# Kernel tuning notes

Hardware: AMD Instinct MI355X
Metric: run time of the kernel (lower is better)

Reference implementation:

```python
import jax, jax.numpy as jnp
import numpy as np

ALPHA = 0.25
GAMMA = 2.0
EPS_CLIP = 1e-4


def calc_iou(a, b):
    # a: [A,4] anchors, b: [M,4] gt boxes, boxes are [x1,y1,x2,y2]
    area = (b[:, 2] - b[:, 0]) * (b[:, 3] - b[:, 1])  # [M]
    iw = jnp.minimum(a[:, None, 2], b[None, :, 2]) - jnp.maximum(a[:, None, 0], b[None, :, 0])
    ih = jnp.minimum(a[:, None, 3], b[None, :, 3]) - jnp.maximum(a[:, None, 1], b[None, :, 1])
    iw = jnp.maximum(iw, 0.0)
    ih = jnp.maximum(ih, 0.0)
    ua = ((a[:, 2] - a[:, 0]) * (a[:, 3] - a[:, 1]))[:, None] + area[None, :] - iw * ih
    ua = jnp.maximum(ua, 1e-8)
    return iw * ih / ua  # [A,M]


def _per_image(cls_p, reg_p, ann, anchor):
    # cls_p [A,C], reg_p [A,4], ann [M,5], anchor [A,4]
    aw = anchor[:, 2] - anchor[:, 0]
    ah = anchor[:, 3] - anchor[:, 1]
    acx = anchor[:, 0] + 0.5 * aw
    acy = anchor[:, 1] + 0.5 * ah

    valid = ann[:, 4] != -1.0            # [M] padding mask
    has_ann = jnp.any(valid)

    cls_p = jnp.clip(cls_p, EPS_CLIP, 1.0 - EPS_CLIP)

    iou = calc_iou(anchor, ann[:, :4])   # [A,M]
    iou = jnp.where(valid[None, :], iou, -1.0)  # invalid gt never matched
    iou_max = jnp.max(iou, axis=1)       # [A]
    iou_arg = jnp.argmax(iou, axis=1)    # [A]
    assigned = ann[iou_arg]              # [A,5]

    neg = iou_max < 0.4
    pos = iou_max >= 0.5
    num_pos = jnp.sum(pos.astype(jnp.float32))

    C = cls_p.shape[1]
    targets = jnp.full_like(cls_p, -1.0)
    targets = jnp.where(neg[:, None], 0.0, targets)
    targets = jnp.where(pos[:, None], 0.0, targets)
    cls_idx = assigned[:, 4].astype(jnp.int32)
    onehot = (jnp.arange(C)[None, :] == cls_idx[:, None]) & pos[:, None]
    targets = jnp.where(onehot, 1.0, targets)

    alpha_f = jnp.where(targets == 1.0, ALPHA, 1.0 - ALPHA)
    focal_w = alpha_f * jnp.where(targets == 1.0, 1.0 - cls_p, cls_p) ** GAMMA
    bce = -(targets * jnp.log(cls_p) + (1.0 - targets) * jnp.log(1.0 - cls_p))
    cls_loss = jnp.where(targets != -1.0, focal_w * bce, 0.0)
    cls_l = jnp.where(has_ann, jnp.sum(cls_loss) / jnp.maximum(num_pos, 1.0), 0.0)

    gw0 = assigned[:, 2] - assigned[:, 0]
    gh0 = assigned[:, 3] - assigned[:, 1]
    gcx = assigned[:, 0] + 0.5 * gw0
    gcy = assigned[:, 1] + 0.5 * gh0
    gw = jnp.maximum(gw0, 1.0)
    gh = jnp.maximum(gh0, 1.0)
    tdx = (gcx - acx) / aw
    tdy = (gcy - acy) / ah
    tdw = jnp.log(gw / aw)
    tdh = jnp.log(gh / ah)
    norm = jnp.array([0.1, 0.1, 0.2, 0.2], dtype=cls_p.dtype)
    rt = jnp.stack([tdx, tdy, tdw, tdh], axis=1) / norm  # [A,4]

    diff = jnp.abs(rt - reg_p)
    sl1 = jnp.where(diff <= 1.0 / 9.0, 0.5 * 9.0 * diff * diff, diff - 0.5 / 9.0)
    reg_sum = jnp.sum(sl1 * pos[:, None].astype(sl1.dtype))
    reg_l = jnp.where(has_ann & (num_pos > 0), reg_sum / jnp.maximum(num_pos * 4.0, 1.0), 0.0)
    return cls_l, reg_l


def setup_inputs() -> dict:
    key = jax.random.key(0)
    ks = jax.random.split(key, 10)
    B, A, C, M = 8, 49104, 90, 32
    IMG = 512.0

    classifications = jax.random.uniform(ks[0], (B, A, C), dtype=jnp.float32)
    regressions = jax.random.normal(ks[1], (B, A, 4), dtype=jnp.float32)

    # anchors: valid boxes [x1,y1,x2,y2]
    acx = jax.random.uniform(ks[2], (A,), minval=0.0, maxval=IMG)
    acy = jax.random.uniform(ks[3], (A,), minval=0.0, maxval=IMG)
    asz = jax.random.uniform(ks[4], (A, 2), minval=16.0, maxval=128.0)
    anchors = jnp.stack([acx - 0.5 * asz[:, 0], acy - 0.5 * asz[:, 1],
                         acx + 0.5 * asz[:, 0], acy + 0.5 * asz[:, 1]], axis=1)[None].astype(jnp.float32)

    # annotations: [x1,y1,x2,y2,label], label=-1 marks padding
    gx1 = jax.random.uniform(ks[5], (B, M), minval=0.0, maxval=IMG - 64.0)
    gy1 = jax.random.uniform(ks[6], (B, M), minval=0.0, maxval=IMG - 64.0)
    gwh = jax.random.uniform(ks[7], (B, M, 2), minval=16.0, maxval=64.0)
    labels = jax.random.randint(ks[8], (B, M), 0, C).astype(jnp.float32)
    invalid = jax.random.uniform(ks[9], (B, M)) < 0.25
    labels = jnp.where(invalid, -1.0, labels)
    labels = labels.at[:, 0].set(jnp.abs(labels[:, 0]))  # ensure >=1 valid gt per image
    annotations = jnp.concatenate([gx1[..., None], gy1[..., None],
                                   (gx1 + gwh[..., 0])[..., None],
                                   (gy1 + gwh[..., 1])[..., None],
                                   labels[..., None]], axis=-1).astype(jnp.float32)

    return {"classifications": classifications, "regressions": regressions,
            "anchors": anchors, "annotations": annotations}


def reference(classifications, regressions, anchors, annotations):
    cls_l, reg_l = jax.vmap(_per_image, in_axes=(0, 0, 0, None))(
        classifications, regressions, annotations, anchors[0])
    return (jnp.mean(cls_l, keepdims=True), jnp.mean(reg_l, keepdims=True))
```

## Files before the change

kernel.cpp:

```cpp
#include <hip/hip_runtime.h>

constexpr int B = 8;
constexpr int A = 49104;
constexpr int C = 90;
constexpr int M = 32;
constexpr float EPS_CLIP = 1e-4f;
constexpr float LN2 = 0.6931471805599453f;

constexpr int APB = 256;
constexpr int TPB = 256;
constexpr int UN  = 8;


__global__ __launch_bounds__(TPB, 6) void focal_fused_kernel(
    const float* __restrict__ cls,
    const float* __restrict__ reg,
    const float* __restrict__ anc,
    const float* __restrict__ ann,
    float* __restrict__ accum)
{
    __shared__ float s_ann[M * 5];
    __shared__ int   s_meta[APB + 1];
    __shared__ float s_red[3][TPB / 64];

    const int b     = blockIdx.y;
    const int abase = blockIdx.x * APB;
    const int t     = threadIdx.x;
    const int nA    = min(APB, A - abase);

    if (t < M * 5) s_ann[t] = ann[b * M * 5 + t];
    __syncthreads();

    float reg_sum = 0.f;
    float pos_cnt = 0.f;
    int   mymeta  = -1;

    if (t < nA) {
        const int a = abase + t;
        const float4 ab = reinterpret_cast<const float4*>(anc)[a];
        const float aw = ab.z - ab.x;
        const float ah = ab.w - ab.y;
        const float areaA = aw * ah;

        float best = -INFINITY;
        int argm = 0;
        for (int m = 0; m < M; ++m) {
            const float bx1 = s_ann[m * 5 + 0];
            const float by1 = s_ann[m * 5 + 1];
            const float bx2 = s_ann[m * 5 + 2];
            const float by2 = s_ann[m * 5 + 3];
            const float lab = s_ann[m * 5 + 4];
            float iw = fminf(ab.z, bx2) - fmaxf(ab.x, bx1);
            float ih = fminf(ab.w, by2) - fmaxf(ab.y, by1);
            iw = fmaxf(iw, 0.f);
            ih = fmaxf(ih, 0.f);
            const float inter = iw * ih;
            const float ua = fmaxf(areaA + (bx2 - bx1) * (by2 - by1) - inter, 1e-8f);
            const float iou = inter / ua;
            const float val = (lab != -1.0f) ? iou : -1.0f;
            if (val > best) { best = val; argm = m; }
        }

        const bool pos = best >= 0.5f;
        const bool neg = best < 0.4f;
        mymeta = pos ? (int)s_ann[argm * 5 + 4] : (neg ? -1 : -2);

        if (pos) {
            pos_cnt = 1.f;
            const float gx1 = s_ann[argm * 5 + 0];
            const float gy1 = s_ann[argm * 5 + 1];
            const float gx2 = s_ann[argm * 5 + 2];
            const float gy2 = s_ann[argm * 5 + 3];
            const float acx = ab.x + 0.5f * aw;
            const float acy = ab.y + 0.5f * ah;
            const float gw0 = gx2 - gx1;
            const float gh0 = gy2 - gy1;
            const float gcx = gx1 + 0.5f * gw0;
            const float gcy = gy1 + 0.5f * gh0;
            const float gw = fmaxf(gw0, 1.f);
            const float gh = fmaxf(gh0, 1.f);
            const float4 rp = reinterpret_cast<const float4*>(reg)[(size_t)b * A + a];
            const float rt0 = (gcx - acx) / aw * 10.f;
            const float rt1 = (gcy - acy) / ah * 10.f;
            const float rt2 = __logf(gw / aw) * 5.f;
            const float rt3 = __logf(gh / ah) * 5.f;
            const float d0 = fabsf(rt0 - rp.x);
            const float d1 = fabsf(rt1 - rp.y);
            const float d2 = fabsf(rt2 - rp.z);
            const float d3 = fabsf(rt3 - rp.w);
            auto sl1 = [](float d) {
                return (d <= (1.f / 9.f)) ? 4.5f * d * d : d - (0.5f / 9.f);
            };
            reg_sum = sl1(d0) + sl1(d1) + sl1(d2) + sl1(d3);
        }
    }
    s_meta[t] = mymeta;
    if (t == 0) s_meta[APB] = -1;
    const int nspecial = __syncthreads_count(mymeta != -1);

    float acc = 0.f;
    const float4* cp = reinterpret_cast<const float4*>(
        cls + ((size_t)b * A + abase) * (size_t)C);
    const int n4 = (nA * C) >> 2;

    if (nspecial == 0) {
        for (int base = t; base < n4; base += UN * TPB) {
            float4 v[UN];
#pragma unroll
            for (int k = 0; k < UN; ++k) {
                const int ix = base + k * TPB;
                v[k] = cp[ix < n4 ? ix : 0];
            }
#pragma unroll
            for (int k = 0; k < UN; ++k) {
                if (base + k * TPB < n4) {
                    const float vv[4] = {v[k].x, v[k].y, v[k].z, v[k].w};
#pragma unroll
                    for (int j = 0; j < 4; ++j) {
                        const float p = fminf(fmaxf(vv[j], EPS_CLIP), 1.f - EPS_CLIP);
                        acc = fmaf(p * p, __log2f(1.f - p), acc);
                    }
                }
            }
        }
        acc *= 0.75f;
    } else {
        for (int base = t; base < n4; base += UN * TPB) {
            float4 v[UN];
#pragma unroll
            for (int k = 0; k < UN; ++k) {
                const int ix = base + k * TPB;
                v[k] = cp[ix < n4 ? ix : 0];
            }
#pragma unroll
            for (int k = 0; k < UN; ++k) {
                const int ix = base + k * TPB;
                if (ix < n4) {
                    const int e  = ix << 2;
                    const int a0 = e / C;
                    const int c0 = e - a0 * C;
                    const int m0 = s_meta[a0];
                    const int m1 = (c0 >= C - 3) ? s_meta[a0 + 1] : m0;
                    const float vv[4] = {v[k].x, v[k].y, v[k].z, v[k].w};
#pragma unroll
                    for (int j = 0; j < 4; ++j) {
                        int cc = c0 + j;
                        int mm = m0;
                        if (cc >= C) { cc -= C; mm = m1; }
                        const float p = fminf(fmaxf(vv[j], EPS_CLIP), 1.f - EPS_CLIP);
                        const bool t1 = (mm == cc);
                        const float parg = t1 ? p : (1.f - p);
                        const float qq   = t1 ? (1.f - p) : p;
                        const float w    = (t1 ? 0.25f : 0.75f) * qq * qq;
                        acc += (mm == -2) ? 0.f : w * __log2f(parg);
                    }
                }
            }
        }
    }

    float v0 = acc, v1 = reg_sum, v2 = pos_cnt;
    for (int off = 32; off; off >>= 1) {
        v0 += __shfl_down(v0, off);
        v1 += __shfl_down(v1, off);
        v2 += __shfl_down(v2, off);
    }
    const int wave = t >> 6;
    const int lane = t & 63;
    if (lane == 0) {
        s_red[0][wave] = v0;
        s_red[1][wave] = v1;
        s_red[2][wave] = v2;
    }
    __syncthreads();
    if (t == 0) {
        float a0 = 0.f, a1 = 0.f, a2 = 0.f;
        for (int w = 0; w < TPB / 64; ++w) {
            a0 += s_red[0][w];
            a1 += s_red[1][w];
            a2 += s_red[2][w];
        }
        atomicAdd(&accum[b],         a0 * (-LN2));
        atomicAdd(&accum[B + b],     a1);
        atomicAdd(&accum[2 * B + b], a2);
    }
}

__global__ void focal_finalize_kernel(const float* __restrict__ ann,
                                      const float* __restrict__ accum,
                                      float* __restrict__ out)
{
    const int t = threadIdx.x;
    float cls_l = 0.f, reg_l = 0.f;
    if (t < B) {
        bool has = false;
        for (int m = 0; m < M; ++m)
            has = has || (ann[t * M * 5 + m * 5 + 4] != -1.0f);
        const float np = accum[2 * B + t];
        const float cs = accum[t];
        const float rs = accum[B + t];
        cls_l = has ? cs / fmaxf(np, 1.f) : 0.f;
        reg_l = (has && np > 0.f) ? rs / fmaxf(np * 4.f, 1.f) : 0.f;
    }
    for (int off = 4; off; off >>= 1) {
        cls_l += __shfl_down(cls_l, off);
        reg_l += __shfl_down(reg_l, off);
    }
    if (t == 0) {
        out[0] = cls_l * (1.f / B);
        out[1] = reg_l * (1.f / B);
    }
}

extern "C" void kernel_launch(void* const* d_in, const int* in_sizes, int n_in,
                              void* d_out, int out_size, void* d_ws, size_t ws_size,
                              hipStream_t stream) {
    const float* cls = (const float*)d_in[0];
    const float* reg = (const float*)d_in[1];
    const float* anc = (const float*)d_in[2];
    const float* ann = (const float*)d_in[3];
    float* out = (float*)d_out;
    float* accum = (float*)d_ws;

    hipMemsetAsync(accum, 0, 3 * B * sizeof(float), stream);

    dim3 grid((A + APB - 1) / APB, B);
    focal_fused_kernel<<<grid, TPB, 0, stream>>>(cls, reg, anc, ann, accum);
    focal_finalize_kernel<<<1, 64, 0, stream>>>(ann, accum, out);
}
```

Baseline: 67.56 us.

## Split focal loss into uniform negative stream plus per-anchor correction kernel

```diff
diff --git a/kernel.cpp b/kernel.cpp
--- a/kernel.cpp
+++ b/kernel.cpp
@@ -7,12 +7,19 @@
 constexpr float EPS_CLIP = 1e-4f;
 constexpr float LN2 = 0.6931471805599453f;
 
-constexpr int APB = 256;
 constexpr int TPB = 256;
-constexpr int UN  = 8;
-
-
-__global__ __launch_bounds__(TPB, 6) void focal_fused_kernel(
+constexpr int UNB = 8;
+constexpr int N4_IMG = A * C / 4;
+constexpr int CHUNK = TPB * UNB;
+constexpr int NCHUNK = (N4_IMG + CHUNK - 1) / CHUNK;
+constexpr int GRIDX_B = 256;
+
+
+__device__ __forceinline__ float clampp(float v) {
+    return fminf(fmaxf(v, EPS_CLIP), 1.f - EPS_CLIP);
+}
+
+__global__ __launch_bounds__(TPB) void focal_anchor_kernel(
     const float* __restrict__ cls,
     const float* __restrict__ reg,
     const float* __restrict__ anc,
@@ -20,23 +27,18 @@
     float* __restrict__ accum)
 {
     __shared__ float s_ann[M * 5];
-    __shared__ int   s_meta[APB + 1];
     __shared__ float s_red[3][TPB / 64];
 
-    const int b     = blockIdx.y;
-    const int abase = blockIdx.x * APB;
-    const int t     = threadIdx.x;
-    const int nA    = min(APB, A - abase);
+    const int b = blockIdx.y;
+    const int abase = blockIdx.x * TPB;
+    const int t = threadIdx.x;
 
     if (t < M * 5) s_ann[t] = ann[b * M * 5 + t];
     __syncthreads();
 
-    float reg_sum = 0.f;
-    float pos_cnt = 0.f;
-    int   mymeta  = -1;
-
-    if (t < nA) {
-        const int a = abase + t;
+    float corr = 0.f, reg_sum = 0.f, pos_cnt = 0.f;
+    const int a = abase + t;
+    if (a < A) {
         const float4 ab = reinterpret_cast<const float4*>(anc)[a];
         const float aw = ab.z - ab.x;
         const float ah = ab.w - ab.y;
@@ -61,11 +63,7 @@
             if (val > best) { best = val; argm = m; }
         }
 
-        const bool pos = best >= 0.5f;
-        const bool neg = best < 0.4f;
-        mymeta = pos ? (int)s_ann[argm * 5 + 4] : (neg ? -1 : -2);
-
-        if (pos) {
+        if (best >= 0.5f) {
             pos_cnt = 1.f;
             const float gx1 = s_ann[argm * 5 + 0];
             const float gy1 = s_ann[argm * 5 + 1];
@@ -92,97 +90,93 @@
                 return (d <= (1.f / 9.f)) ? 4.5f * d * d : d - (0.5f / 9.f);
             };
             reg_sum = sl1(d0) + sl1(d1) + sl1(d2) + sl1(d3);
+
+            const int cidx = (int)s_ann[argm * 5 + 4];
+            const float p = clampp(cls[((size_t)b * A + a) * C + cidx]);
+            corr = 0.75f * LN2 * (p * p * __log2f(1.f - p))
+                 + 0.25f * (1.f - p) * (1.f - p) * (-__logf(p));
+        } else if (best >= 0.4f) {
+            const float* row = cls + ((size_t)b * A + a) * C;
+            float s = 0.f;
+            for (int c = 0; c < C; ++c) {
+                const float p = clampp(row[c]);
+                s = fmaf(p * p, __log2f(1.f - p), s);
+            }
+            corr = 0.75f * LN2 * s;
         }
     }
-    s_meta[t] = mymeta;
-    if (t == 0) s_meta[APB] = -1;
-    const int nspecial = __syncthreads_count(mymeta != -1);
-
-    float acc = 0.f;
-    const float4* cp = reinterpret_cast<const float4*>(
-        cls + ((size_t)b * A + abase) * (size_t)C);
-    const int n4 = (nA * C) >> 2;
-
-    if (nspecial == 0) {
-        for (int base = t; base < n4; base += UN * TPB) {
-            float4 v[UN];
-#pragma unroll
-            for (int k = 0; k < UN; ++k) {
-                const int ix = base + k * TPB;
-                v[k] = cp[ix < n4 ? ix : 0];
-            }
-#pragma unroll
-            for (int k = 0; k < UN; ++k) {
-                if (base + k * TPB < n4) {
-                    const float vv[4] = {v[k].x, v[k].y, v[k].z, v[k].w};
-#pragma unroll
-                    for (int j = 0; j < 4; ++j) {
-                        const float p = fminf(fmaxf(vv[j], EPS_CLIP), 1.f - EPS_CLIP);
-                        acc = fmaf(p * p, __log2f(1.f - p), acc);
-                    }
-                }
-            }
-        }
-        acc *= 0.75f;
-    } else {
-        for (int base = t; base < n4; base += UN * TPB) {
-            float4 v[UN];
-#pragma unroll
-            for (int k = 0; k < UN; ++k) {
-                const int ix = base + k * TPB;
-                v[k] = cp[ix < n4 ? ix : 0];
-            }
-#pragma unroll
-            for (int k = 0; k < UN; ++k) {
-                const int ix = base + k * TPB;
-                if (ix < n4) {
-                    const int e  = ix << 2;
-                    const int a0 = e / C;
-                    const int c0 = e - a0 * C;
-                    const int m0 = s_meta[a0];
-                    const int m1 = (c0 >= C - 3) ? s_meta[a0 + 1] : m0;
-                    const float vv[4] = {v[k].x, v[k].y, v[k].z, v[k].w};
-#pragma unroll
-                    for (int j = 0; j < 4; ++j) {
-                        int cc = c0 + j;
-                        int mm = m0;
-                        if (cc >= C) { cc -= C; mm = m1; }
-                        const float p = fminf(fmaxf(vv[j], EPS_CLIP), 1.f - EPS_CLIP);
-                        const bool t1 = (mm == cc);
-                        const float parg = t1 ? p : (1.f - p);
-                        const float qq   = t1 ? (1.f - p) : p;
-                        const float w    = (t1 ? 0.25f : 0.75f) * qq * qq;
-                        acc += (mm == -2) ? 0.f : w * __log2f(parg);
-                    }
-                }
-            }
-        }
-    }
-
-    float v0 = acc, v1 = reg_sum, v2 = pos_cnt;
+
+    float v0 = corr, v1 = reg_sum, v2 = pos_cnt;
     for (int off = 32; off; off >>= 1) {
         v0 += __shfl_down(v0, off);
         v1 += __shfl_down(v1, off);
         v2 += __shfl_down(v2, off);
     }
     const int wave = t >> 6;
-    const int lane = t & 63;
-    if (lane == 0) {
-        s_red[0][wave] = v0;
-        s_red[1][wave] = v1;
-        s_red[2][wave] = v2;
-    }
+    if ((t & 63) == 0) { s_red[0][wave] = v0; s_red[1][wave] = v1; s_red[2][wave] = v2; }
     __syncthreads();
     if (t == 0) {
         float a0 = 0.f, a1 = 0.f, a2 = 0.f;
-        for (int w = 0; w < TPB / 64; ++w) {
-            a0 += s_red[0][w];
-            a1 += s_red[1][w];
-            a2 += s_red[2][w];
+        for (int w = 0; w < TPB / 64; ++w) { a0 += s_red[0][w]; a1 += s_red[1][w]; a2 += s_red[2][w]; }
+        atomicAdd(&accum[B + b],     a0);
+        atomicAdd(&accum[2 * B + b], a1);
+        atomicAdd(&accum[3 * B + b], a2);
+    }
+}
+
+__global__ __launch_bounds__(TPB) void focal_neg_stream_kernel(
+    const float* __restrict__ cls,
+    float* __restrict__ accum)
+{
+    __shared__ float s_red[TPB / 64];
+    const int b = blockIdx.y;
+    const int t = threadIdx.x;
+    const float4* __restrict__ cp = reinterpret_cast<const float4*>(cls) + (size_t)b * N4_IMG;
+
+    float acc = 0.f;
+    for (int c = blockIdx.x; c < NCHUNK; c += GRIDX_B) {
+        const int base = c * CHUNK + t;
+        if ((c + 1) * CHUNK <= N4_IMG) {
+            float4 v[UNB];
+#pragma unroll
+            for (int k = 0; k < UNB; ++k) v[k] = cp[base + k * TPB];
+#pragma unroll
+            for (int k = 0; k < UNB; ++k) {
+                const float vv[4] = {v[k].x, v[k].y, v[k].z, v[k].w};
+#pragma unroll
+                for (int j = 0; j < 4; ++j) {
+                    const float p = clampp(vv[j]);
+                    acc = fmaf(p * p, __log2f(1.f - p), acc);
+                }
+            }
+        } else {
+            float4 v[UNB];
+#pragma unroll
+            for (int k = 0; k < UNB; ++k) {
+                const int ix = base + k * TPB;
+                v[k] = cp[ix < N4_IMG ? ix : 0];
+            }
+#pragma unroll
+            for (int k = 0; k < UNB; ++k) {
+                if (base + k * TPB < N4_IMG) {
+                    const float vv[4] = {v[k].x, v[k].y, v[k].z, v[k].w};
+#pragma unroll
+                    for (int j = 0; j < 4; ++j) {
+                        const float p = clampp(vv[j]);
+                        acc = fmaf(p * p, __log2f(1.f - p), acc);
+                    }
+                }
+            }
         }
-        atomicAdd(&accum[b],         a0 * (-LN2));
-        atomicAdd(&accum[B + b],     a1);
-        atomicAdd(&accum[2 * B + b], a2);
+    }
+
+    for (int off = 32; off; off >>= 1) acc += __shfl_down(acc, off);
+    if ((t & 63) == 0) s_red[t >> 6] = acc;
+    __syncthreads();
+    if (t == 0) {
+        float a0 = 0.f;
+        for (int w = 0; w < TPB / 64; ++w) a0 += s_red[w];
+        atomicAdd(&accum[b], a0);
     }
 }
 
@@ -196,10 +190,12 @@
         bool has = false;
         for (int m = 0; m < M; ++m)
             has = has || (ann[t * M * 5 + m * 5 + 4] != -1.0f);
-        const float np = accum[2 * B + t];
-        const float cs = accum[t];
-        const float rs = accum[B + t];
-        cls_l = has ? cs / fmaxf(np, 1.f) : 0.f;
+        const float S    = accum[t];
+        const float corr = accum[B + t];
+        const float rs   = accum[2 * B + t];
+        const float np   = accum[3 * B + t];
+        const float cls_sum = -0.75f * LN2 * S + corr;
+        cls_l = has ? cls_sum / fmaxf(np, 1.f) : 0.f;
         reg_l = (has && np > 0.f) ? rs / fmaxf(np * 4.f, 1.f) : 0.f;
     }
     for (int off = 4; off; off >>= 1) {
@@ -222,9 +218,13 @@
     float* out = (float*)d_out;
     float* accum = (float*)d_ws;
 
-    hipMemsetAsync(accum, 0, 3 * B * sizeof(float), stream);
-
-    dim3 grid((A + APB - 1) / APB, B);
-    focal_fused_kernel<<<grid, TPB, 0, stream>>>(cls, reg, anc, ann, accum);
+    hipMemsetAsync(accum, 0, 4 * B * sizeof(float), stream);
+
+    dim3 gridA((A + TPB - 1) / TPB, B);
+    focal_anchor_kernel<<<gridA, TPB, 0, stream>>>(cls, reg, anc, ann, accum);
+
+    dim3 gridB(GRIDX_B, B);
+    focal_neg_stream_kernel<<<gridB, TPB, 0, stream>>>(cls, accum);
+
     focal_finalize_kernel<<<1, 64, 0, stream>>>(ann, accum, out);
 }
```

New measurement: 97.33 us. 1.44x slower.
